# Kernel optimization log

Hardware: AMD Instinct MI355X
Metric: run time of the kernel (lower is better)

The kernel has to match this reference:

```python
import jax, jax.numpy as jnp
import numpy as np

MIN_DEPTH = 0.1
MAX_DEPTH = 100.0
EPS = 1e-10


def setup_inputs() -> dict:
    key = jax.random.key(0)
    k1, k2, k3 = jax.random.split(key, 3)
    B, R, S = 4, 16384, 128
    colors = jax.random.uniform(k1, (B, R, S, 3), dtype=jnp.float32)
    density_logits = jax.random.normal(k2, (B, R, S, 1), dtype=jnp.float32)
    # depths must be monotonically increasing along the sample axis
    depths = jnp.sort(jax.random.uniform(k3, (B, R, S, 1), dtype=jnp.float32) * 50.0, axis=2)
    return {"colors": colors, "density_logits": density_logits, "depths": depths}


def reference(colors, density_logits, depths):
    # midpoints along the sample axis (dim 2)
    colors_mid = (colors[:, :, :-1] + colors[:, :, 1:]) * 0.5          # [B,R,S-1,3]
    dl_mid = (density_logits[:, :, :-1] + density_logits[:, :, 1:]) * 0.5
    depths_mid = (depths[:, :, :-1] + depths[:, :, 1:]) * 0.5          # [B,R,S-1,1]
    deltas = depths[:, :, 1:] - depths[:, :, :-1]

    # density_activation == 'softplus'
    densities_mid = jax.nn.softplus(dl_mid - 1.0)

    alpha = 1.0 - jnp.exp(-densities_mid * deltas)                     # [B,R,S-1,1]
    alpha_shifted = jnp.concatenate(
        [jnp.ones_like(alpha[:, :, :1]), 1.0 - alpha + EPS], axis=-2)
    transmittance = jnp.cumprod(alpha_shifted, axis=-2)[:, :, :-1]
    weights = (alpha + EPS) * transmittance                            # [B,R,S-1,1]
    weight_total = weights.sum(axis=2)                                 # [B,R,1]

    # c_sky is None branch
    weights_all = weights
    composite_rgb = jnp.sum(weights * colors_mid, axis=-2)             # [B,R,3]
    composite_depth = jnp.sum(weights * depths_mid, axis=-2) / (EPS + weight_total)

    composite_depth = jnp.nan_to_num(composite_depth, nan=MAX_DEPTH)
    composite_depth = jnp.clip(composite_depth, MIN_DEPTH, MAX_DEPTH)
    composite_rgb = composite_rgb * 2.0 - 1.0
    return (composite_rgb, composite_depth, weights, weights_all, alpha, depths_mid)
```

## Files before the change

kernel.cpp:

```cpp
#include <hip/hip_runtime.h>
#include <math.h>

namespace {
constexpr int Bn = 4, Rn = 16384, Sn = 128;
constexpr int NRAY = Bn * Rn;
constexpr int SI   = Sn - 1;
constexpr size_t OFF_RGB   = 0;
constexpr size_t OFF_DEPTH = OFF_RGB   + (size_t)NRAY * 3;
constexpr size_t OFF_W     = OFF_DEPTH + (size_t)NRAY;
constexpr size_t OFF_WALL  = OFF_W     + (size_t)NRAY * SI;
constexpr size_t OFF_ALPHA = OFF_WALL  + (size_t)NRAY * SI;
constexpr size_t OFF_DMID  = OFF_ALPHA + (size_t)NRAY * SI;
constexpr float  EPSF      = 1e-10f;
}

__global__ __launch_bounds__(256) void raymarch_kernel(
    const float* __restrict__ colors,
    const float* __restrict__ dlog,
    const float* __restrict__ depths,
    float* __restrict__ out)
{
    const int gtid = blockIdx.x * 256 + threadIdx.x;
    const int ray  = gtid >> 6;
    const int lane = threadIdx.x & 63;

    const float2* dp = reinterpret_cast<const float2*>(depths) + (size_t)ray * (Sn / 2);
    const float2* gp = reinterpret_cast<const float2*>(dlog)   + (size_t)ray * (Sn / 2);
    const float2* cp = reinterpret_cast<const float2*>(colors) + (size_t)ray * (Sn * 3 / 2);

    float2 d  = dp[lane];
    float2 g  = gp[lane];
    float2 c0 = cp[lane * 3 + 0];
    float2 c1 = cp[lane * 3 + 1];
    float2 c2 = cp[lane * 3 + 2];

    float d2  = __shfl_down(d.x, 1);
    float g2  = __shfl_down(g.x, 1);
    float cnx = __shfl_down(c0.x, 1);
    float cny = __shfl_down(c0.y, 1);
    float cnz = __shfl_down(c1.x, 1);

    const bool valid1 = (lane < 63);

    float delta0 = d.y - d.x;
    float dm0    = 0.5f * (d.x + d.y);
    float x0     = 0.5f * (g.x + g.y) - 1.0f;
    float cm0x   = 0.5f * (c0.x + c1.y);
    float cm0y   = 0.5f * (c0.y + c2.x);
    float cm0z   = 0.5f * (c1.x + c2.y);

    float delta1 = valid1 ? (d2 - d.y)            : 0.0f;
    float dm1    = valid1 ? 0.5f * (d.y + d2)     : 0.0f;
    float x1     = valid1 ? (0.5f * (g.y + g2) - 1.0f) : 0.0f;
    float cm1x   = valid1 ? 0.5f * (c1.y + cnx)   : 0.0f;
    float cm1y   = valid1 ? 0.5f * (c2.x + cny)   : 0.0f;
    float cm1z   = valid1 ? 0.5f * (c2.y + cnz)   : 0.0f;

    float dens0 = fmaxf(x0, 0.0f) + log1pf(expf(-fabsf(x0)));
    float dens1 = fmaxf(x1, 0.0f) + log1pf(expf(-fabsf(x1)));
    float alpha0 = 1.0f - expf(-dens0 * delta0);
    float alpha1 = 1.0f - expf(-dens1 * delta1);
    float t0 = 1.0f - alpha0 + EPSF;
    float t1 = valid1 ? (1.0f - alpha1 + EPSF) : 1.0f;

    float s = t0 * t1;
    #pragma unroll
    for (int off = 1; off < 64; off <<= 1) {
        float y = __shfl_up(s, off);
        if (lane >= off) s *= y;
    }
    float T0 = __shfl_up(s, 1);
    if (lane == 0) T0 = 1.0f;
    float T1 = T0 * t0;

    float w0 = (alpha0 + EPSF) * T0;
    float w1 = valid1 ? (alpha1 + EPSF) * T1 : 0.0f;

    size_t base = (size_t)ray * SI + 2 * lane;
    out[OFF_W     + base] = w0;
    out[OFF_WALL  + base] = w0;
    out[OFF_ALPHA + base] = alpha0;
    out[OFF_DMID  + base] = dm0;
    if (valid1) {
        out[OFF_W     + base + 1] = w1;
        out[OFF_WALL  + base + 1] = w1;
        out[OFF_ALPHA + base + 1] = alpha1;
        out[OFF_DMID  + base + 1] = dm1;
    }

    float wsum = w0 + w1;
    float rx = w0 * cm0x + w1 * cm1x;
    float ry = w0 * cm0y + w1 * cm1y;
    float rz = w0 * cm0z + w1 * cm1z;
    float dsum = w0 * dm0 + w1 * dm1;
    #pragma unroll
    for (int m = 32; m > 0; m >>= 1) {
        wsum += __shfl_xor(wsum, m);
        rx   += __shfl_xor(rx, m);
        ry   += __shfl_xor(ry, m);
        rz   += __shfl_xor(rz, m);
        dsum += __shfl_xor(dsum, m);
    }
    if (lane == 0) {
        float cd = dsum / (EPSF + wsum);
        if (isnan(cd)) cd = 100.0f;
        cd = fminf(fmaxf(cd, 0.1f), 100.0f);
        out[OFF_RGB + (size_t)ray * 3 + 0] = rx * 2.0f - 1.0f;
        out[OFF_RGB + (size_t)ray * 3 + 1] = ry * 2.0f - 1.0f;
        out[OFF_RGB + (size_t)ray * 3 + 2] = rz * 2.0f - 1.0f;
        out[OFF_DEPTH + ray] = cd;
    }
}

extern "C" void kernel_launch(void* const* d_in, const int* in_sizes, int n_in,
                              void* d_out, int out_size, void* d_ws, size_t ws_size,
                              hipStream_t stream) {
    const float* colors = (const float*)d_in[0];
    const float* dlog   = (const float*)d_in[1];
    const float* depths = (const float*)d_in[2];
    float* out = (float*)d_out;

    dim3 grid(NRAY / 4);
    dim3 block(256);
    hipLaunchKernelGGL(raymarch_kernel, grid, block, 0, stream, colors, dlog, depths, out);
}
```

Baseline: 262.0 us.

## Replace wave shuffles with DPP scans, use fast softplus math, nontemporal stores

Replaces the ds_bpermute-based shuffles (neighbor fetch, prefix product, xor reductions) with DPP row shifts and row broadcasts. The scan and the reductions now finish in lane 63. Softplus and alpha are rewritten in log2/exp2 form using fast intrinsics, and transmittance is taken directly as exp(-x) instead of 1-alpha. Output stores become nontemporal. This cuts LDS-path cross-lane traffic and transcendental cost, but the kernel is likely memory-bound, and the fast math and wave_shr row_mask semantics may change accuracy or correctness.

```diff
diff --git a/kernel.cpp b/kernel.cpp
--- a/kernel.cpp
+++ b/kernel.cpp
@@ -12,6 +12,32 @@
 constexpr size_t OFF_ALPHA = OFF_WALL  + (size_t)NRAY * SI;
 constexpr size_t OFF_DMID  = OFF_ALPHA + (size_t)NRAY * SI;
 constexpr float  EPSF      = 1e-10f;
+}
+
+template<int CTRL, int ROW_MASK, bool BC>
+__device__ __forceinline__ float dpp_mov(float oldv, float src) {
+    return __int_as_float(__builtin_amdgcn_update_dpp(
+        __float_as_int(oldv), __float_as_int(src), CTRL, ROW_MASK, 0xF, BC));
+}
+
+__device__ __forceinline__ float wave_prefix_prod(float s) {
+    s *= dpp_mov<0x111, 0xF, false>(1.0f, s);
+    s *= dpp_mov<0x112, 0xF, false>(1.0f, s);
+    s *= dpp_mov<0x114, 0xF, false>(1.0f, s);
+    s *= dpp_mov<0x118, 0xF, false>(1.0f, s);
+    s *= dpp_mov<0x142, 0xa, false>(1.0f, s);
+    s *= dpp_mov<0x143, 0xc, false>(1.0f, s);
+    return s;
+}
+
+__device__ __forceinline__ float wave_sum_last(float x) {
+    x += dpp_mov<0x111, 0xF, true>(0.0f, x);
+    x += dpp_mov<0x112, 0xF, true>(0.0f, x);
+    x += dpp_mov<0x114, 0xF, true>(0.0f, x);
+    x += dpp_mov<0x118, 0xF, true>(0.0f, x);
+    x += dpp_mov<0x142, 0xa, true>(0.0f, x);
+    x += dpp_mov<0x143, 0xc, true>(0.0f, x);
+    return x;
 }
 
 __global__ __launch_bounds__(256) void raymarch_kernel(
@@ -34,11 +60,11 @@
     float2 c1 = cp[lane * 3 + 1];
     float2 c2 = cp[lane * 3 + 2];
 
-    float d2  = __shfl_down(d.x, 1);
-    float g2  = __shfl_down(g.x, 1);
-    float cnx = __shfl_down(c0.x, 1);
-    float cny = __shfl_down(c0.y, 1);
-    float cnz = __shfl_down(c1.x, 1);
+    float d2  = dpp_mov<0x130, 0xF, false>(d.x,  d.x);
+    float g2  = dpp_mov<0x130, 0xF, false>(g.x,  g.x);
+    float cnx = dpp_mov<0x130, 0xF, false>(c0.x, c0.x);
+    float cny = dpp_mov<0x130, 0xF, false>(c0.y, c0.y);
+    float cnz = dpp_mov<0x130, 0xF, false>(c1.x, c1.x);
 
     const bool valid1 = (lane < 63);
 
@@ -56,52 +82,43 @@
     float cm1y   = valid1 ? 0.5f * (c2.x + cny)   : 0.0f;
     float cm1z   = valid1 ? 0.5f * (c2.y + cnz)   : 0.0f;
 
-    float dens0 = fmaxf(x0, 0.0f) + log1pf(expf(-fabsf(x0)));
-    float dens1 = fmaxf(x1, 0.0f) + log1pf(expf(-fabsf(x1)));
-    float alpha0 = 1.0f - expf(-dens0 * delta0);
-    float alpha1 = 1.0f - expf(-dens1 * delta1);
-    float t0 = 1.0f - alpha0 + EPSF;
-    float t1 = valid1 ? (1.0f - alpha1 + EPSF) : 1.0f;
+    float l0 = __log2f(1.0f + __expf(x0));
+    float l1 = __log2f(1.0f + __expf(x1));
+    l0 = fminf(l0, 1e30f);
+    l1 = fminf(l1, 1e30f);
+    float E0 = exp2f(-delta0 * l0);
+    float E1 = exp2f(-delta1 * l1);
+    float alpha0 = 1.0f - E0;
+    float alpha1 = 1.0f - E1;
+    float t0 = E0 + EPSF;
+    float t1 = valid1 ? (E1 + EPSF) : 1.0f;
 
-    float s = t0 * t1;
-    #pragma unroll
-    for (int off = 1; off < 64; off <<= 1) {
-        float y = __shfl_up(s, off);
-        if (lane >= off) s *= y;
-    }
-    float T0 = __shfl_up(s, 1);
-    if (lane == 0) T0 = 1.0f;
+    float s  = wave_prefix_prod(t0 * t1);
+    float T0 = dpp_mov<0x138, 0xF, false>(1.0f, s);
     float T1 = T0 * t0;
 
     float w0 = (alpha0 + EPSF) * T0;
     float w1 = valid1 ? (alpha1 + EPSF) * T1 : 0.0f;
 
     size_t base = (size_t)ray * SI + 2 * lane;
-    out[OFF_W     + base] = w0;
-    out[OFF_WALL  + base] = w0;
-    out[OFF_ALPHA + base] = alpha0;
-    out[OFF_DMID  + base] = dm0;
+    __builtin_nontemporal_store(w0,     out + OFF_W     + base);
+    __builtin_nontemporal_store(w0,     out + OFF_WALL  + base);
+    __builtin_nontemporal_store(alpha0, out + OFF_ALPHA + base);
+    __builtin_nontemporal_store(dm0,    out + OFF_DMID  + base);
     if (valid1) {
-        out[OFF_W     + base + 1] = w1;
-        out[OFF_WALL  + base + 1] = w1;
-        out[OFF_ALPHA + base + 1] = alpha1;
-        out[OFF_DMID  + base + 1] = dm1;
+        __builtin_nontemporal_store(w1,     out + OFF_W     + base + 1);
+        __builtin_nontemporal_store(w1,     out + OFF_WALL  + base + 1);
+        __builtin_nontemporal_store(alpha1, out + OFF_ALPHA + base + 1);
+        __builtin_nontemporal_store(dm1,    out + OFF_DMID  + base + 1);
     }
 
-    float wsum = w0 + w1;
-    float rx = w0 * cm0x + w1 * cm1x;
-    float ry = w0 * cm0y + w1 * cm1y;
-    float rz = w0 * cm0z + w1 * cm1z;
-    float dsum = w0 * dm0 + w1 * dm1;
-    #pragma unroll
-    for (int m = 32; m > 0; m >>= 1) {
-        wsum += __shfl_xor(wsum, m);
-        rx   += __shfl_xor(rx, m);
-        ry   += __shfl_xor(ry, m);
-        rz   += __shfl_xor(rz, m);
-        dsum += __shfl_xor(dsum, m);
-    }
-    if (lane == 0) {
+    float wsum = wave_sum_last(w0 + w1);
+    float rx   = wave_sum_last(w0 * cm0x + w1 * cm1x);
+    float ry   = wave_sum_last(w0 * cm0y + w1 * cm1y);
+    float rz   = wave_sum_last(w0 * cm0z + w1 * cm1z);
+    float dsum = wave_sum_last(w0 * dm0  + w1 * dm1);
+
+    if (lane == 63) {
         float cd = dsum / (EPSF + wsum);
         if (isnan(cd)) cd = 100.0f;
         cd = fminf(fmaxf(cd, 0.1f), 100.0f);
```

Result: slower. 331.8 us (+26.7%).
